# Kernel optimization log

Measured on AMD Instinct MI355X. Metric: run time of the kernel, lower is better.

Reference implementation:

```python
import jax, jax.numpy as jnp
import numpy as np

B, C, H, W = 2, 192, 64, 64
NHEADS = 8


def setup_inputs() -> dict:
    key = jax.random.key(0)
    ks = jax.random.split(key, 6)
    L = H * W
    return {
        "x": jax.random.normal(ks[0], (B, C, H, W), dtype=jnp.float32),
        "mask": jax.random.normal(ks[1], (B, L, L), dtype=jnp.float32),
        "w_qkv": jax.random.normal(ks[2], (3 * C, C), dtype=jnp.float32) * (1.0 / np.sqrt(C)),
        "b_qkv": jax.random.normal(ks[3], (3 * C,), dtype=jnp.float32) * 0.02,
        "w_proj": jax.random.normal(ks[4], (C, C), dtype=jnp.float32) * (1.0 / np.sqrt(C)),
        "b_proj": jax.random.normal(ks[5], (C,), dtype=jnp.float32) * 0.02,
        "num_heads": NHEADS,
    }


def reference(x, mask, w_qkv, b_qkv, w_proj, b_proj, num_heads):
    b, c, h, w = x.shape
    L = h * w
    hd = c // num_heads  # head dim
    # 1x1 conv == per-pixel linear over channels
    qkv = jnp.einsum('bchw,oc->bohw', x, w_qkv) + b_qkv[None, :, None, None]
    q, k, v = jnp.split(qkv, 3, axis=1)  # each [b, c, h, w]

    def to_heads(t):
        # b (head hd) h w -> b head (h w) hd
        return t.reshape(b, num_heads, hd, L).transpose(0, 1, 3, 2)

    q, k, v = to_heads(q), to_heads(k), to_heads(v)
    scale = num_heads ** (-0.5)  # NOTE: original scales by num_heads, not head_dim
    attn = jnp.einsum('bnld,bnmd->bnlm', q, k) * scale + mask[:, None, :, :]
    attn = jax.nn.softmax(attn, axis=-1)
    out = jnp.einsum('bnlm,bnmd->bnld', attn, v)  # [b, head, L, hd]
    # b head L hd -> b (head hd) h w
    out = out.transpose(0, 1, 3, 2).reshape(b, c, h, w)
    out = jnp.einsum('bchw,oc->bohw', out, w_proj) + b_proj[None, :, None, None]
    return out
```

## Files before the change

kernel.cpp:

```cpp
#include <hip/hip_runtime.h>

#define B_  2
#define C_  192
#define L_  4096
#define NH_ 8
#define HD_ 24
#define C3_ 576
#define KV_ 64
#define NSPL_ 2
#define LSPL_ (L_ / NSPL_)
#define NT2_ (LSPL_ / KV_)

typedef _Float16 f16;
typedef __attribute__((ext_vector_type(8))) f16 f16x8;
typedef __attribute__((ext_vector_type(16))) float f32x16;

#define L2E_ 1.4426950408889634f

__device__ __forceinline__ int pk2(float a, float b) {
    union { __fp16 h __attribute__((ext_vector_type(2))); int i; } u;
    u.h = __builtin_amdgcn_cvt_pkrtz(a, b);
    return u.i;
}
__device__ __forceinline__ int pk2_rte(float a, float b) {
    union { f16 h[2]; int i; } u;
    u.h[0] = (f16)a; u.h[1] = (f16)b;
    return u.i;
}
__device__ __forceinline__ float ex2(float x) {
    float r;
    asm("v_exp_f32 %0, %1" : "=v"(r) : "v"(x));
    return r;
}
__device__ __forceinline__ float lg2(float x) {
    float r;
    asm("v_log_f32 %0, %1" : "=v"(r) : "v"(x));
    return r;
}

union Frag { f16x8 v; int i[4]; };

#define MFMA32(A, Bx, Cc) __builtin_amdgcn_mfma_f32_32x32x16_f16((A), (Bx), (Cc), 0, 0, 0)

__device__ __forceinline__ void gload4(const void* g, void* lds) {
    typedef const unsigned int __attribute__((address_space(1))) as1u;
    typedef unsigned int __attribute__((address_space(3))) as3u;
    __builtin_amdgcn_global_load_lds((as1u*)g,
                                     (as3u*)(unsigned int)(unsigned long long)lds,
                                     4, 0, 0);
}

__global__ __launch_bounds__(256) void lin_qkv(const float* __restrict__ a,
                                               const float* __restrict__ w,
                                               const float* __restrict__ bias,
                                               unsigned int* __restrict__ q2,
                                               unsigned int* __restrict__ k2,
                                               unsigned short* __restrict__ v16) {
    __shared__ float wl[8][C_];
    const int og  = blockIdx.x;
    const int b   = blockIdx.y >> 4;
    const int lt  = blockIdx.y & 15;
    const int tid = threadIdx.x;

    for (int e = tid; e < 8 * C_; e += 256) wl[e / C_][e % C_] = w[og * 8 * C_ + e];
    __syncthreads();

    const int l = lt * 256 + tid;
    float acc[8];
#pragma unroll
    for (int j = 0; j < 8; ++j) acc[j] = bias[og * 8 + j];

    const float* ap = a + (size_t)b * C_ * L_ + l;
#pragma unroll 2
    for (int c = 0; c < C_; ++c) {
        const float xv = ap[(size_t)c * L_];
#pragma unroll
        for (int j = 0; j < 8; ++j) acc[j] = fmaf(wl[j][c], xv, acc[j]);
    }

    const float qscale = 0.35355339059327373f * L2E_;
    if (og < 48) {
        unsigned int* dst = (og < 24) ? q2 : k2;
        const int og_ = (og < 24) ? og : og - 24;
        const float sc = (og < 24) ? qscale : 1.f;
        const int h = og_ / 3, j0 = (og_ % 3) * 4;
        unsigned int* p = dst + ((size_t)(b * NH_ + h) * 12 + j0) * L_ + l;
#pragma unroll
        for (int j = 0; j < 4; ++j)
            p[(size_t)j * L_] = pk2_rte(acc[2 * j] * sc, acc[2 * j + 1] * sc);
    } else {
        const int og_ = og - 48;
        const int h = og_ / 3, d0 = (og_ % 3) * 8;
        unsigned short* p = v16 + ((size_t)(b * NH_ + h) * 24 + d0) * L_ + l;
#pragma unroll
        for (int j = 0; j < 8; ++j) {
            union { f16 hf; unsigned short us; } cv;
            cv.hf = (f16)acc[j];
            p[(size_t)j * L_] = cv.us;
        }
    }
}

__global__ __launch_bounds__(256) void lin_kernel(const float* __restrict__ a,
                                                  const float* __restrict__ w,
                                                  const float* __restrict__ bias,
                                                  float* __restrict__ out, int OC) {
    __shared__ float wl[8][C_];
    const int og  = blockIdx.x;
    const int b   = blockIdx.y >> 4;
    const int lt  = blockIdx.y & 15;
    const int tid = threadIdx.x;

    for (int e = tid; e < 8 * C_; e += 256) wl[e / C_][e % C_] = w[og * 8 * C_ + e];
    __syncthreads();

    const int l = lt * 256 + tid;
    float acc[8];
#pragma unroll
    for (int j = 0; j < 8; ++j) acc[j] = bias[og * 8 + j];

    const float* ap = a + (size_t)b * C_ * L_ + l;
#pragma unroll 2
    for (int c = 0; c < C_; ++c) {
        const float xv = ap[(size_t)c * L_];
#pragma unroll
        for (int j = 0; j < 8; ++j) acc[j] = fmaf(wl[j][c], xv, acc[j]);
    }

    float* op = out + ((size_t)b * OC + og * 8) * L_ + l;
#pragma unroll
    for (int j = 0; j < 8; ++j) op[(size_t)j * L_] = acc[j];
}

__global__ __launch_bounds__(256) void attn_mfma(const unsigned int* __restrict__ q2,
                                                 const unsigned int* __restrict__ k2,
                                                 const unsigned short* __restrict__ v16,
                                                 const float* __restrict__ mask,
                                                 unsigned short* __restrict__ po,
                                                 float* __restrict__ pms) {
    const int tid  = threadIdx.x;
    const int lane = tid & 63;
    const int wid  = tid >> 6;
    const int hi   = lane >> 5;
    const int lq   = lane & 31;
    const int bid  = blockIdx.x;
    const int sp   = bid >> 9;
    const int r    = bid & 511;
    const int h    = r >> 6;
    const int b    = (r >> 5) & 1;
    const int qt   = r & 31;
    const int qrow = qt * 128 + wid * 32 + lq;
    const int kv0  = sp * LSPL_;

    __shared__ int k_lds[2][16][64];
    __shared__ int v_lds[2][32][32];

    {
        const int rr = 12 + (tid >> 6), cc = tid & 63;
        k_lds[0][rr][cc] = 0;
        k_lds[1][rr][cc] = 0;
    }

    const unsigned int*   qb = q2  + (size_t)(b * NH_ + h) * 12 * L_;
    const unsigned int*   kb = k2  + (size_t)(b * NH_ + h) * 12 * L_;
    const unsigned short* vb = v16 + (size_t)(b * NH_ + h) * 24 * L_;
    const float* mrow = mask + ((size_t)b * L_ + qrow) * L_;

    int bq[8];
#pragma unroll
    for (int s = 0; s < 2; ++s)
#pragma unroll
        for (int t = 0; t < 4; ++t) {
            const int dpq = 8 * s + 4 * hi + t;
            bq[s * 4 + t] = (dpq < 12) ? qb[(size_t)dpq * L_ + qrow] : 0;
        }

    const unsigned int*   kg[3];
    const unsigned short* vg[3];
    int ls_off[3];
#pragma unroll
    for (int i = 0; i < 3; ++i) {
        const int e = i * 256 + tid;
        kg[i]     = kb + (size_t)(e >> 6) * L_ + (e & 63);
        const int d = e >> 5, slot = e & 31;
        vg[i]     = vb + (size_t)d * L_ + 2 * (slot ^ d);
        ls_off[i] = i * 256 + 64 * wid;
    }

#define STAGE(BF, KK) do {                                                    \
    _Pragma("unroll")                                                         \
    for (int i_ = 0; i_ < 3; ++i_) {                                          \
        gload4(kg[i_] + (KK), &k_lds[BF][0][0] + ls_off[i_]);                 \
        gload4(vg[i_] + (KK), &v_lds[BF][0][0] + ls_off[i_]);                 \
    } } while (0)

#define MLOAD(MD, KK) do {                                                    \
    const float4* mb_ = (const float4*)(mrow + (KK));                         \
    _Pragma("unroll")                                                         \
    for (int u_ = 0; u_ < 2; ++u_)                                            \
        _Pragma("unroll")                                                     \
        for (int q_ = 0; q_ < 4; ++q_)                                        \
            MD[u_ * 4 + q_] = mb_[8 * u_ + 2 * q_ + hi];                      \
    } while (0)

#define PVSTEP(BF, CU, U) do {                                                \
    int w1[4], w2[4], s1[4], s2[4];                                           \
    _Pragma("unroll")                                                         \
    for (int q_ = 0; q_ < 4; ++q_) {                                          \
        w1[q_] = pk2(CU[4 * q_], CU[4 * q_ + 1]);                             \
        w2[q_] = pk2(CU[4 * q_ + 2], CU[4 * q_ + 3]);                         \
    }                                                                         \
    _Pragma("unroll")                                                         \
    for (int q_ = 0; q_ < 4; ++q_) {                                          \
        s1[q_] = __shfl_xor(w1[q_], 32);                                      \
        s2[q_] = __shfl_xor(w2[q_], 32);                                      \
    }                                                                         \
    _Pragma("unroll")                                                         \
    for (int s_ = 0; s_ < 2; ++s_) {                                          \
        const int qq_ = 2 * s_ + hi;                                          \
        Frag pb, va;                                                          \
        pb.i[0] = hi ? s1[qq_] : w1[qq_];                                     \
        pb.i[1] = hi ? s2[qq_] : w2[qq_];                                     \
        pb.i[2] = hi ? w1[qq_] : s1[qq_];                                     \
        pb.i[3] = hi ? w2[qq_] : s2[qq_];                                     \
        _Pragma("unroll")                                                     \
        for (int t_ = 0; t_ < 4; ++t_)                                        \
            va.i[t_] = v_lds[BF][lq][(16 * U + 8 * s_ + 4 * hi + t_) ^ lq];   \
        __builtin_amdgcn_s_setprio(1);                                        \
        o = MFMA32(va.v, pb.v, o);                                            \
        __builtin_amdgcn_s_setprio(0);                                        \
    } } while (0)

#define COMPUTE(BF, MC) do {                                                  \
    f32x16 c0, c1;                                                            \
    c0[0]  = MC[0].x * L2E_; c0[1]  = MC[0].y * L2E_;                         \
    c0[2]  = MC[0].z * L2E_; c0[3]  = MC[0].w * L2E_;                         \
    c0[4]  = MC[1].x * L2E_; c0[5]  = MC[1].y * L2E_;                         \
    c0[6]  = MC[1].z * L2E_; c0[7]  = MC[1].w * L2E_;                         \
    c0[8]  = MC[2].x * L2E_; c0[9]  = MC[2].y * L2E_;                         \
    c0[10] = MC[2].z * L2E_; c0[11] = MC[2].w * L2E_;                         \
    c0[12] = MC[3].x * L2E_; c0[13] = MC[3].y * L2E_;                         \
    c0[14] = MC[3].z * L2E_; c0[15] = MC[3].w * L2E_;                         \
    c1[0]  = MC[4].x * L2E_; c1[1]  = MC[4].y * L2E_;                         \
    c1[2]  = MC[4].z * L2E_; c1[3]  = MC[4].w * L2E_;                         \
    c1[4]  = MC[5].x * L2E_; c1[5]  = MC[5].y * L2E_;                         \
    c1[6]  = MC[5].z * L2E_; c1[7]  = MC[5].w * L2E_;                         \
    c1[8]  = MC[6].x * L2E_; c1[9]  = MC[6].y * L2E_;                         \
    c1[10] = MC[6].z * L2E_; c1[11] = MC[6].w * L2E_;                         \
    c1[12] = MC[7].x * L2E_; c1[13] = MC[7].y * L2E_;                         \
    c1[14] = MC[7].z * L2E_; c1[15] = MC[7].w * L2E_;                         \
    Frag qf0, qf1, ka0, ka1;                                                  \
    _Pragma("unroll")                                                         \
    for (int t_ = 0; t_ < 4; ++t_) { qf0.i[t_] = bq[t_]; qf1.i[t_] = bq[4 + t_]; } \
    _Pragma("unroll")                                                         \
    for (int t_ = 0; t_ < 4; ++t_) {                                          \
        ka0.i[t_] = k_lds[BF][4 * hi + t_][lq];                               \
        ka1.i[t_] = k_lds[BF][8 + 4 * hi + t_][lq];                           \
    }                                                                         \
    __builtin_amdgcn_s_setprio(1);                                            \
    c0 = MFMA32(ka0.v, qf0.v, c0);                                            \
    c0 = MFMA32(ka1.v, qf1.v, c0);                                            \
    __builtin_amdgcn_s_setprio(0);                                            \
    _Pragma("unroll")                                                         \
    for (int t_ = 0; t_ < 4; ++t_) {                                          \
        ka0.i[t_] = k_lds[BF][4 * hi + t_][32 + lq];                          \
        ka1.i[t_] = k_lds[BF][8 + 4 * hi + t_][32 + lq];                      \
    }                                                                         \
    __builtin_amdgcn_s_setprio(1);                                            \
    c1 = MFMA32(ka0.v, qf0.v, c1);                                            \
    c1 = MFMA32(ka1.v, qf1.v, c1);                                            \
    __builtin_amdgcn_s_setprio(0);                                            \
    float pmax = c0[0];                                                       \
    _Pragma("unroll")                                                         \
    for (int i_ = 1; i_ < 16; ++i_) pmax = fmaxf(pmax, c0[i_]);               \
    _Pragma("unroll")                                                         \
    for (int i_ = 0; i_ < 16; ++i_) pmax = fmaxf(pmax, c1[i_]);               \
    pmax = fmaxf(pmax, __shfl_xor(pmax, 32));                                 \
    if (!__all((int)(pmax <= mrun + 11.5415603f))) {                          \
        const float newm_ = fmaxf(mrun, pmax);                                \
        const float r_ = ex2(mrun - newm_);                                   \
        srun *= r_;                                                           \
        _Pragma("unroll")                                                     \
        for (int i_ = 0; i_ < 16; ++i_) o[i_] *= r_;                          \
        mrun = newm_;                                                         \
    }                                                                         \
    float ls = 0.f;                                                           \
    _Pragma("unroll")                                                         \
    for (int i_ = 0; i_ < 16; ++i_) { c0[i_] = ex2(c0[i_] - mrun); ls += c0[i_]; } \
    _Pragma("unroll")                                                         \
    for (int i_ = 0; i_ < 16; ++i_) { c1[i_] = ex2(c1[i_] - mrun); ls += c1[i_]; } \
    ls += __shfl_xor(ls, 32);                                                 \
    srun += ls;                                                               \
    PVSTEP(BF, c0, 0);                                                        \
    PVSTEP(BF, c1, 1);                                                        \
    } while (0)

    f32x16 o;
#pragma unroll
    for (int i = 0; i < 16; ++i) o[i] = 0.f;
    float mrun = -1e30f, srun = 0.f;
    float4 mc[8], mn[8];

    STAGE(0, kv0);
    MLOAD(mc, kv0);
    __syncthreads();

    for (int t = 0; t < NT2_; t += 2) {
        const int kk = kv0 + t * KV_;
        STAGE(1, kk + KV_);
        MLOAD(mn, kk + KV_);
        COMPUTE(0, mc);
        __syncthreads();
        if (t + 2 < NT2_) {
            STAGE(0, kk + 2 * KV_);
            MLOAD(mc, kk + 2 * KV_);
        }
        COMPUTE(1, mn);
        __syncthreads();
    }

    const float inv = 1.f / srun;
    const float lse = mrun + lg2(srun);
    unsigned short* pob = po + ((size_t)((sp * B_ + b) * NH_ + h) * HD_) * L_ + qrow;
#pragma unroll
    for (int i = 0; i < 16; ++i) {
        const int d = (i & 3) + 8 * (i >> 2) + 4 * hi;
        if (d < HD_) {
            union { __fp16 hf; unsigned short us; } cv;
            cv.hf = (__fp16)(o[i] * inv);
            pob[(size_t)d * L_] = cv.us;
        }
    }
    if (hi == 0)
        pms[((size_t)(sp * B_ + b) * NH_ + h) * L_ + qrow] = lse;
#undef STAGE
#undef MLOAD
#undef PVSTEP
#undef COMPUTE
}

__global__ __launch_bounds__(256) void combine_kernel(const unsigned short* __restrict__ po,
                                                      const float* __restrict__ pms,
                                                      float* __restrict__ att) {
    const int qrow = blockIdx.x * 256 + threadIdx.x;
    const int h    = blockIdx.y;
    const int b    = blockIdx.z;

    const float l0 = pms[((size_t)(0 * B_ + b) * NH_ + h) * L_ + qrow];
    const float l1 = pms[((size_t)(1 * B_ + b) * NH_ + h) * L_ + qrow];
    const float lm = fmaxf(l0, l1);
    const float w0 = ex2(l0 - lm);
    const float w1 = ex2(l1 - lm);
    const float inv = 1.f / (w0 + w1);

    const unsigned short* p0 = po + ((size_t)((0 * B_ + b) * NH_ + h) * HD_) * L_ + qrow;
    const unsigned short* p1 = po + ((size_t)((1 * B_ + b) * NH_ + h) * HD_) * L_ + qrow;
    float* op = att + ((size_t)b * C_ + h * HD_) * L_ + qrow;
#pragma unroll
    for (int d = 0; d < HD_; ++d) {
        union { unsigned short us; __fp16 hf; } a, c;
        a.us = p0[(size_t)d * L_];
        c.us = p1[(size_t)d * L_];
        op[(size_t)d * L_] = ((float)a.hf * w0 + (float)c.hf * w1) * inv;
    }
}

extern "C" void kernel_launch(void* const* d_in, const int* in_sizes, int n_in,
                              void* d_out, int out_size, void* d_ws, size_t ws_size,
                              hipStream_t stream) {
    const float* x      = (const float*)d_in[0];
    const float* mask   = (const float*)d_in[1];
    const float* w_qkv  = (const float*)d_in[2];
    const float* b_qkv  = (const float*)d_in[3];
    const float* w_proj = (const float*)d_in[4];
    const float* b_proj = (const float*)d_in[5];
    float* out = (float*)d_out;

    unsigned int*   q2  = (unsigned int*)d_ws;
    unsigned int*   k2  = q2 + (size_t)B_ * NH_ * 12 * L_;
    unsigned short* v16 = (unsigned short*)(k2 + (size_t)B_ * NH_ * 12 * L_);
    unsigned short* po  = v16 + (size_t)B_ * NH_ * HD_ * L_;
    float* pms    = (float*)(po + (size_t)NSPL_ * B_ * NH_ * HD_ * L_);
    float* ws_att = pms + (size_t)NSPL_ * B_ * NH_ * L_;

    lin_qkv<<<dim3(72, 32), 256, 0, stream>>>(x, w_qkv, b_qkv, q2, k2, v16);
    attn_mfma<<<dim3(512 * NSPL_), 256, 0, stream>>>(q2, k2, v16, mask, po, pms);
    combine_kernel<<<dim3(16, NH_, B_), 256, 0, stream>>>(po, pms, ws_att);
    lin_kernel<<<dim3(24, 32), 256, 0, stream>>>(ws_att, w_proj, b_proj, out, C_);
}
```

Baseline: 345.0 us.

## Process four heads per block to reuse mask loads across heads

Each attention block now handles four heads for the same query rows and batch, so every mask tile loaded from global memory feeds four heads instead of one. This cuts the dominant mask traffic, which is shared across heads. To keep the grid at 512 blocks, the KV split grows from two to four, and the combine kernel becomes generic over the split count. Each wave stages K/V for its own head with wider 16-byte LDS loads. The costs are more registers (four accumulators and Q fragments per thread), more shared memory, and more partial results to write and merge.

```diff
diff --git a/kernel.cpp b/kernel.cpp
--- a/kernel.cpp
+++ b/kernel.cpp
@@ -7,9 +7,10 @@
 #define HD_ 24
 #define C3_ 576
 #define KV_ 64
-#define NSPL_ 2
+#define NSPL_ 4
 #define LSPL_ (L_ / NSPL_)
-#define NT2_ (LSPL_ / KV_)
+#define NTS_ (LSPL_ / KV_)
+#define HG_ 4
 
 typedef _Float16 f16;
 typedef __attribute__((ext_vector_type(8))) f16 f16x8;
@@ -48,6 +49,13 @@
     __builtin_amdgcn_global_load_lds((as1u*)g,
                                      (as3u*)(unsigned int)(unsigned long long)lds,
                                      4, 0, 0);
+}
+__device__ __forceinline__ void gload16(const void* g, void* lds) {
+    typedef const unsigned int __attribute__((address_space(1))) as1u;
+    typedef unsigned int __attribute__((address_space(3))) as3u;
+    __builtin_amdgcn_global_load_lds((as1u*)g,
+                                     (as3u*)(unsigned int)(unsigned long long)lds,
+                                     16, 0, 0);
 }
 
 __global__ __launch_bounds__(256) void lin_qkv(const float* __restrict__ a,
@@ -144,66 +152,97 @@
     const int hi   = lane >> 5;
     const int lq   = lane & 31;
     const int bid  = blockIdx.x;
-    const int sp   = bid >> 9;
-    const int r    = bid & 511;
-    const int h    = r >> 6;
-    const int b    = (r >> 5) & 1;
-    const int qt   = r & 31;
+    const int qt   = bid & 31;
+    const int r    = bid >> 5;
+    const int b    = r & 1;
+    const int hg   = (r >> 1) & 1;
+    const int sp   = r >> 2;
     const int qrow = qt * 128 + wid * 32 + lq;
     const int kv0  = sp * LSPL_;
-
-    __shared__ int k_lds[2][16][64];
-    __shared__ int v_lds[2][32][32];
-
-    {
-        const int rr = 12 + (tid >> 6), cc = tid & 63;
-        k_lds[0][rr][cc] = 0;
-        k_lds[1][rr][cc] = 0;
-    }
-
-    const unsigned int*   qb = q2  + (size_t)(b * NH_ + h) * 12 * L_;
-    const unsigned int*   kb = k2  + (size_t)(b * NH_ + h) * 12 * L_;
-    const unsigned short* vb = v16 + (size_t)(b * NH_ + h) * 24 * L_;
+    const int hbase = hg * HG_;
+
+    __shared__ int k_lds[2][HG_][16][64];
+    __shared__ int v_lds[2][HG_][32][32];
+
+#pragma unroll
+    for (int z = 0; z < 8; ++z) {
+        const int wd = z * 256 + tid;
+        k_lds[wd >> 10][(wd >> 8) & 3][12 + ((wd >> 6) & 3)][wd & 63] = 0;
+    }
+
+    const unsigned int*   qb   = q2  + (size_t)(b * NH_ + hbase) * 12 * L_;
+    const unsigned int*   kb_w = k2  + (size_t)(b * NH_ + hbase + wid) * 12 * L_;
+    const unsigned short* vb_w = v16 + (size_t)(b * NH_ + hbase + wid) * 24 * L_;
     const float* mrow = mask + ((size_t)b * L_ + qrow) * L_;
 
-    int bq[8];
-#pragma unroll
-    for (int s = 0; s < 2; ++s)
-#pragma unroll
-        for (int t = 0; t < 4; ++t) {
-            const int dpq = 8 * s + 4 * hi + t;
-            bq[s * 4 + t] = (dpq < 12) ? qb[(size_t)dpq * L_ + qrow] : 0;
-        }
-
-    const unsigned int*   kg[3];
-    const unsigned short* vg[3];
-    int ls_off[3];
-#pragma unroll
-    for (int i = 0; i < 3; ++i) {
-        const int e = i * 256 + tid;
-        kg[i]     = kb + (size_t)(e >> 6) * L_ + (e & 63);
-        const int d = e >> 5, slot = e & 31;
-        vg[i]     = vb + (size_t)d * L_ + 2 * (slot ^ d);
-        ls_off[i] = i * 256 + 64 * wid;
-    }
+    int bq[HG_][8];
+#pragma unroll
+    for (int H = 0; H < HG_; ++H)
+#pragma unroll
+        for (int s = 0; s < 2; ++s)
+#pragma unroll
+            for (int t = 0; t < 4; ++t) {
+                const int dpq = 8 * s + 4 * hi + t;
+                bq[H][s * 4 + t] = (dpq < 12) ? qb[(size_t)(H * 12 + dpq) * L_ + qrow] : 0;
+            }
 
 #define STAGE(BF, KK) do {                                                    \
     _Pragma("unroll")                                                         \
-    for (int i_ = 0; i_ < 3; ++i_) {                                          \
-        gload4(kg[i_] + (KK), &k_lds[BF][0][0] + ls_off[i_]);                 \
-        gload4(vg[i_] + (KK), &v_lds[BF][0][0] + ls_off[i_]);                 \
+    for (int j_ = 0; j_ < 3; ++j_) {                                          \
+        const int dp_ = j_ * 4 + (lane >> 4);                                 \
+        gload16(kb_w + (size_t)dp_ * L_ + (KK) + 4 * (lane & 15),             \
+                &k_lds[BF][wid][0][0] + j_ * 256);                            \
+    }                                                                         \
+    _Pragma("unroll")                                                         \
+    for (int j_ = 0; j_ < 12; ++j_) {                                         \
+        const int e_ = j_ * 64 + lane;                                        \
+        const int d_ = e_ >> 5, sl_ = e_ & 31;                                \
+        gload4(vb_w + (size_t)d_ * L_ + (KK) + 2 * (sl_ ^ d_),                \
+               &v_lds[BF][wid][0][0] + j_ * 64);                              \
     } } while (0)
 
-#define MLOAD(MD, KK) do {                                                    \
+#define MLOADX(KK) do {                                                       \
     const float4* mb_ = (const float4*)(mrow + (KK));                         \
     _Pragma("unroll")                                                         \
-    for (int u_ = 0; u_ < 2; ++u_)                                            \
-        _Pragma("unroll")                                                     \
-        for (int q_ = 0; q_ < 4; ++q_)                                        \
-            MD[u_ * 4 + q_] = mb_[8 * u_ + 2 * q_ + hi];                      \
+    for (int q_ = 0; q_ < 4; ++q_) {                                          \
+        const float4 t0_ = mb_[2 * q_ + hi];                                  \
+        mr0[4 * q_ + 0] = t0_.x; mr0[4 * q_ + 1] = t0_.y;                     \
+        mr0[4 * q_ + 2] = t0_.z; mr0[4 * q_ + 3] = t0_.w;                     \
+        const float4 t1_ = mb_[8 + 2 * q_ + hi];                              \
+        mr1[4 * q_ + 0] = t1_.x; mr1[4 * q_ + 1] = t1_.y;                     \
+        mr1[4 * q_ + 2] = t1_.z; mr1[4 * q_ + 3] = t1_.w;                     \
+    } } while (0)
+
+#define MSCALE do {                                                           \
+    _Pragma("unroll")                                                         \
+    for (int i_ = 0; i_ < 16; ++i_) { mr0[i_] *= L2E_; mr1[i_] *= L2E_; }     \
     } while (0)
 
-#define PVSTEP(BF, CU, U) do {                                                \
+#define QKH(H, BF) do {                                                       \
+    Frag qf0, qf1, ka0, ka1;                                                  \
+    _Pragma("unroll")                                                         \
+    for (int t_ = 0; t_ < 4; ++t_) { qf0.i[t_] = bq[H][t_]; qf1.i[t_] = bq[H][4 + t_]; } \
+    _Pragma("unroll")                                                         \
+    for (int t_ = 0; t_ < 4; ++t_) {                                          \
+        ka0.i[t_] = k_lds[BF][H][4 * hi + t_][lq];                            \
+        ka1.i[t_] = k_lds[BF][H][8 + 4 * hi + t_][lq];                        \
+    }                                                                         \
+    __builtin_amdgcn_s_setprio(1);                                            \
+    c0 = MFMA32(ka0.v, qf0.v, mr0);                                           \
+    c0 = MFMA32(ka1.v, qf1.v, c0);                                            \
+    __builtin_amdgcn_s_setprio(0);                                            \
+    _Pragma("unroll")                                                         \
+    for (int t_ = 0; t_ < 4; ++t_) {                                          \
+        ka0.i[t_] = k_lds[BF][H][4 * hi + t_][32 + lq];                       \
+        ka1.i[t_] = k_lds[BF][H][8 + 4 * hi + t_][32 + lq];                   \
+    }                                                                         \
+    __builtin_amdgcn_s_setprio(1);                                            \
+    c1 = MFMA32(ka0.v, qf0.v, mr1);                                           \
+    c1 = MFMA32(ka1.v, qf1.v, c1);                                            \
+    __builtin_amdgcn_s_setprio(0);                                            \
+    } while (0)
+
+#define PVSTEP(BF, H, CU, U) do {                                             \
     int w1[4], w2[4], s1[4], s2[4];                                           \
     _Pragma("unroll")                                                         \
     for (int q_ = 0; q_ < 4; ++q_) {                                          \
@@ -225,118 +264,91 @@
         pb.i[3] = hi ? w2[qq_] : s2[qq_];                                     \
         _Pragma("unroll")                                                     \
         for (int t_ = 0; t_ < 4; ++t_)                                        \
-            va.i[t_] = v_lds[BF][lq][(16 * U + 8 * s_ + 4 * hi + t_) ^ lq];   \
+            va.i[t_] = v_lds[BF][H][lq][(16 * U + 8 * s_ + 4 * hi + t_) ^ lq]; \
         __builtin_amdgcn_s_setprio(1);                                        \
-        o = MFMA32(va.v, pb.v, o);                                            \
+        o[H] = MFMA32(va.v, pb.v, o[H]);                                      \
         __builtin_amdgcn_s_setprio(0);                                        \
     } } while (0)
 
-#define COMPUTE(BF, MC) do {                                                  \
-    f32x16 c0, c1;                                                            \
-    c0[0]  = MC[0].x * L2E_; c0[1]  = MC[0].y * L2E_;                         \
-    c0[2]  = MC[0].z * L2E_; c0[3]  = MC[0].w * L2E_;                         \
-    c0[4]  = MC[1].x * L2E_; c0[5]  = MC[1].y * L2E_;                         \
-    c0[6]  = MC[1].z * L2E_; c0[7]  = MC[1].w * L2E_;                         \
-    c0[8]  = MC[2].x * L2E_; c0[9]  = MC[2].y * L2E_;                         \
-    c0[10] = MC[2].z * L2E_; c0[11] = MC[2].w * L2E_;                         \
-    c0[12] = MC[3].x * L2E_; c0[13] = MC[3].y * L2E_;                         \
-    c0[14] = MC[3].z * L2E_; c0[15] = MC[3].w * L2E_;                         \
-    c1[0]  = MC[4].x * L2E_; c1[1]  = MC[4].y * L2E_;                         \
-    c1[2]  = MC[4].z * L2E_; c1[3]  = MC[4].w * L2E_;                         \
-    c1[4]  = MC[5].x * L2E_; c1[5]  = MC[5].y * L2E_;                         \
-    c1[6]  = MC[5].z * L2E_; c1[7]  = MC[5].w * L2E_;                         \
-    c1[8]  = MC[6].x * L2E_; c1[9]  = MC[6].y * L2E_;                         \
-    c1[10] = MC[6].z * L2E_; c1[11] = MC[6].w * L2E_;                         \
-    c1[12] = MC[7].x * L2E_; c1[13] = MC[7].y * L2E_;                         \
-    c1[14] = MC[7].z * L2E_; c1[15] = MC[7].w * L2E_;                         \
-    Frag qf0, qf1, ka0, ka1;                                                  \
-    _Pragma("unroll")                                                         \
-    for (int t_ = 0; t_ < 4; ++t_) { qf0.i[t_] = bq[t_]; qf1.i[t_] = bq[4 + t_]; } \
-    _Pragma("unroll")                                                         \
-    for (int t_ = 0; t_ < 4; ++t_) {                                          \
-        ka0.i[t_] = k_lds[BF][4 * hi + t_][lq];                               \
-        ka1.i[t_] = k_lds[BF][8 + 4 * hi + t_][lq];                           \
-    }                                                                         \
-    __builtin_amdgcn_s_setprio(1);                                            \
-    c0 = MFMA32(ka0.v, qf0.v, c0);                                            \
-    c0 = MFMA32(ka1.v, qf1.v, c0);                                            \
-    __builtin_amdgcn_s_setprio(0);                                            \
-    _Pragma("unroll")                                                         \
-    for (int t_ = 0; t_ < 4; ++t_) {                                          \
-        ka0.i[t_] = k_lds[BF][4 * hi + t_][32 + lq];                          \
-        ka1.i[t_] = k_lds[BF][8 + 4 * hi + t_][32 + lq];                      \
-    }                                                                         \
-    __builtin_amdgcn_s_setprio(1);                                            \
-    c1 = MFMA32(ka0.v, qf0.v, c1);                                            \
-    c1 = MFMA32(ka1.v, qf1.v, c1);                                            \
-    __builtin_amdgcn_s_setprio(0);                                            \
+#define SMPV(H, BF) do {                                                      \
     float pmax = c0[0];                                                       \
     _Pragma("unroll")                                                         \
     for (int i_ = 1; i_ < 16; ++i_) pmax = fmaxf(pmax, c0[i_]);               \
     _Pragma("unroll")                                                         \
     for (int i_ = 0; i_ < 16; ++i_) pmax = fmaxf(pmax, c1[i_]);               \
     pmax = fmaxf(pmax, __shfl_xor(pmax, 32));                                 \
-    if (!__all((int)(pmax <= mrun + 11.5415603f))) {                          \
-        const float newm_ = fmaxf(mrun, pmax);                                \
-        const float r_ = ex2(mrun - newm_);                                   \
-        srun *= r_;                                                           \
+    if (!__all((int)(pmax <= mrun[H] + 11.5415603f))) {                       \
+        const float newm_ = fmaxf(mrun[H], pmax);                             \
+        const float r_ = ex2(mrun[H] - newm_);                                \
+        srun[H] *= r_;                                                        \
         _Pragma("unroll")                                                     \
-        for (int i_ = 0; i_ < 16; ++i_) o[i_] *= r_;                          \
-        mrun = newm_;                                                         \
+        for (int i_ = 0; i_ < 16; ++i_) o[H][i_] *= r_;                       \
+        mrun[H] = newm_;                                                      \
     }                                                                         \
     float ls = 0.f;                                                           \
     _Pragma("unroll")                                                         \
-    for (int i_ = 0; i_ < 16; ++i_) { c0[i_] = ex2(c0[i_] - mrun); ls += c0[i_]; } \
-    _Pragma("unroll")                                                         \
-    for (int i_ = 0; i_ < 16; ++i_) { c1[i_] = ex2(c1[i_] - mrun); ls += c1[i_]; } \
+    for (int i_ = 0; i_ < 16; ++i_) { c0[i_] = ex2(c0[i_] - mrun[H]); ls += c0[i_]; } \
+    _Pragma("unroll")                                                         \
+    for (int i_ = 0; i_ < 16; ++i_) { c1[i_] = ex2(c1[i_] - mrun[H]); ls += c1[i_]; } \
     ls += __shfl_xor(ls, 32);                                                 \
-    srun += ls;                                                               \
-    PVSTEP(BF, c0, 0);                                                        \
-    PVSTEP(BF, c1, 1);                                                        \
+    srun[H] += ls;                                                            \
+    PVSTEP(BF, H, c0, 0);                                                     \
+    PVSTEP(BF, H, c1, 1);                                                     \
     } while (0)
 
-    f32x16 o;
-#pragma unroll
-    for (int i = 0; i < 16; ++i) o[i] = 0.f;
-    float mrun = -1e30f, srun = 0.f;
-    float4 mc[8], mn[8];
+    f32x16 o[HG_];
+    float mrun[HG_], srun[HG_];
+#pragma unroll
+    for (int H = 0; H < HG_; ++H) {
+#pragma unroll
+        for (int i = 0; i < 16; ++i) o[H][i] = 0.f;
+        mrun[H] = -1e30f;
+        srun[H] = 0.f;
+    }
+    f32x16 mr0, mr1, c0, c1;
 
     STAGE(0, kv0);
-    MLOAD(mc, kv0);
+    MLOADX(kv0);
     __syncthreads();
 
-    for (int t = 0; t < NT2_; t += 2) {
+#pragma clang loop unroll(disable)
+    for (int t = 0; t < NTS_; ++t) {
         const int kk = kv0 + t * KV_;
-        STAGE(1, kk + KV_);
-        MLOAD(mn, kk + KV_);
-        COMPUTE(0, mc);
+        const int cur = t & 1;
+        if (t + 1 < NTS_) STAGE(cur ^ 1, kk + KV_);
+        MSCALE;
+        QKH(0, cur); SMPV(0, cur);
+        QKH(1, cur); SMPV(1, cur);
+        QKH(2, cur); SMPV(2, cur);
+        QKH(3, cur);
+        if (t + 1 < NTS_) MLOADX(kk + KV_);
+        SMPV(3, cur);
         __syncthreads();
-        if (t + 2 < NT2_) {
-            STAGE(0, kk + 2 * KV_);
-            MLOAD(mc, kk + 2 * KV_);
+    }
+
+#pragma unroll
+    for (int H = 0; H < HG_; ++H) {
+        const float inv = 1.f / srun[H];
+        const float lse = mrun[H] + lg2(srun[H]);
+        unsigned short* pob = po + ((size_t)((sp * B_ + b) * NH_ + hbase + H) * HD_) * L_ + qrow;
+#pragma unroll
+        for (int i = 0; i < 16; ++i) {
+            const int d = (i & 3) + 8 * (i >> 2) + 4 * hi;
+            if (d < HD_) {
+                union { __fp16 hf; unsigned short us; } cv;
+                cv.hf = (__fp16)(o[H][i] * inv);
+                pob[(size_t)d * L_] = cv.us;
+            }
         }
-        COMPUTE(1, mn);
-        __syncthreads();
-    }
-
-    const float inv = 1.f / srun;
-    const float lse = mrun + lg2(srun);
-    unsigned short* pob = po + ((size_t)((sp * B_ + b) * NH_ + h) * HD_) * L_ + qrow;
-#pragma unroll
-    for (int i = 0; i < 16; ++i) {
-        const int d = (i & 3) + 8 * (i >> 2) + 4 * hi;
-        if (d < HD_) {
-            union { __fp16 hf; unsigned short us; } cv;
-            cv.hf = (__fp16)(o[i] * inv);
-            pob[(size_t)d * L_] = cv.us;
-        }
-    }
-    if (hi == 0)
-        pms[((size_t)(sp * B_ + b) * NH_ + h) * L_ + qrow] = lse;
+        if (hi == 0)
+            pms[((size_t)(sp * B_ + b) * NH_ + hbase + H) * L_ + qrow] = lse;
+    }
 #undef STAGE
-#undef MLOAD
+#undef MLOADX
+#undef MSCALE
+#undef QKH
 #undef PVSTEP
-#undef COMPUTE
+#undef SMPV
 }
 
 __global__ __launch_bounds__(256) void combine_kernel(const unsigned short* __restrict__ po,
@@ -346,22 +358,29 @@
     const int h    = blockIdx.y;
     const int b    = blockIdx.z;
 
-    const float l0 = pms[((size_t)(0 * B_ + b) * NH_ + h) * L_ + qrow];
-    const float l1 = pms[((size_t)(1 * B_ + b) * NH_ + h) * L_ + qrow];
-    const float lm = fmaxf(l0, l1);
-    const float w0 = ex2(l0 - lm);
-    const float w1 = ex2(l1 - lm);
-    const float inv = 1.f / (w0 + w1);
-
-    const unsigned short* p0 = po + ((size_t)((0 * B_ + b) * NH_ + h) * HD_) * L_ + qrow;
-    const unsigned short* p1 = po + ((size_t)((1 * B_ + b) * NH_ + h) * HD_) * L_ + qrow;
+    float l[NSPL_];
+#pragma unroll
+    for (int s = 0; s < NSPL_; ++s)
+        l[s] = pms[((size_t)(s * B_ + b) * NH_ + h) * L_ + qrow];
+    float lm = l[0];
+#pragma unroll
+    for (int s = 1; s < NSPL_; ++s) lm = fmaxf(lm, l[s]);
+    float wv[NSPL_], wsum = 0.f;
+#pragma unroll
+    for (int s = 0; s < NSPL_; ++s) { wv[s] = ex2(l[s] - lm); wsum += wv[s]; }
+    const float inv = 1.f / wsum;
+
     float* op = att + ((size_t)b * C_ + h * HD_) * L_ + qrow;
 #pragma unroll
     for (int d = 0; d < HD_; ++d) {
-        union { unsigned short us; __fp16 hf; } a, c;
-        a.us = p0[(size_t)d * L_];
-        c.us = p1[(size_t)d * L_];
-        op[(size_t)d * L_] = ((float)a.hf * w0 + (float)c.hf * w1) * inv;
+        float acc = 0.f;
+#pragma unroll
+        for (int s = 0; s < NSPL_; ++s) {
+            union { unsigned short us; __fp16 hf; } cv;
+            cv.us = po[(((size_t)(s * B_ + b) * NH_ + h) * HD_ + d) * L_ + qrow];
+            acc += (float)cv.hf * wv[s];
+        }
+        op[(size_t)d * L_] = acc * inv;
     }
 }
 
@@ -384,7 +403,7 @@
     float* ws_att = pms + (size_t)NSPL_ * B_ * NH_ * L_;
 
     lin_qkv<<<dim3(72, 32), 256, 0, stream>>>(x, w_qkv, b_qkv, q2, k2, v16);
-    attn_mfma<<<dim3(512 * NSPL_), 256, 0, stream>>>(q2, k2, v16, mask, po, pms);
+    attn_mfma<<<dim3(512), 256, 0, stream>>>(q2, k2, v16, mask, po, pms);
     combine_kernel<<<dim3(16, NH_, B_), 256, 0, stream>>>(po, pms, ws_att);
     lin_kernel<<<dim3(24, 32), 256, 0, stream>>>(ws_att, w_proj, b_proj, out, C_);
 }
```

Result: slower. 363.7 us (+5.4%).
